# Kernel tuning notes

Hardware: AMD Instinct MI355X
Metric: run time of the kernel (lower is better)

## Reference

```python
import jax, jax.numpy as jnp
import numpy as np

SIGMA_S = 1.0
SIGMA_R = 0.1
FR = int(np.ceil(3 * SIGMA_S))          # 3
K_SIZE = 2 * FR + 1                     # 7
B, C, H, W = 8, 3, 512, 512


def matlab_style_gauss2d(shape, sigma):
    m, n = [(ss - 1.0) / 2.0 for ss in shape]
    y, x = np.ogrid[-m:m + 1, -n:n + 1]
    h = np.exp(-(x * x + y * y) / (2.0 * sigma * sigma))
    h[h < np.finfo(h.dtype).eps * h.max()] = 0
    s = h.sum()
    if s != 0:
        h /= s
    return h.astype(np.float32)


GAUSS = matlab_style_gauss2d((K_SIZE, K_SIZE), SIGMA_S)  # [7,7]


def setup_inputs() -> dict:
    key = jax.random.key(0)
    x = jax.random.uniform(key, (B, C, H, W), dtype=jnp.float32)
    return {"input": x}


def reference(input) -> jnp.ndarray:
    # ReflectionPad2d(fr)
    padded = jnp.pad(input, ((0, 0), (0, 0), (FR, FR), (FR, FR)), mode="reflect")
    inv_2sr2 = 1.0 / (2.0 * SIGMA_R * SIGMA_R)
    loss_map = jnp.zeros_like(input)
    for k in range(K_SIZE):
        for l in range(K_SIZE):
            shifted = padded[:, :, k:k + H, l:l + W]            # [B,C,H,W]
            d = input - shifted
            # bilateral range weight * gaussian spatial weight (constant, as in
            # the original which stores weight_map as a raw non-grad tensor)
            w = jax.lax.stop_gradient(
                jnp.exp(-(d * d).sum(1, keepdims=True) * inv_2sr2) * GAUSS[k, l]
            )                                                    # [B,1,H,W]
            loss_map = loss_map + jnp.abs(d) * w
    return loss_map.mean()
```

## Files before the change

kernel.cpp:

```cpp
#include <hip/hip_runtime.h>

#define FR 3
#define KS 7
#define TLX 64
#define TLY 16
#define PPT 4
#define HX (TLX + 2*FR)
#define HY (TLY + 2*FR)
#define LSTR 72
#define IMG_H 512
#define IMG_W 512
#define NB 8
#define NC 3
#define GX (IMG_W / TLX)
#define GY (IMG_H / TLY)
#define NBLK (GX * GY * NB)

#define KSC 8.493218f

__device__ __forceinline__ int refl(int i, int n) {
    i = (i < 0) ? -i : i;
    return (i >= n) ? (2*n - 2 - i) : i;
}

__global__ __launch_bounds__(256) void blt_kernel(const float* __restrict__ in,
                                                  float* __restrict__ partial) {
    __shared__ float sm[NC][HY][LSTR];
    __shared__ float gtab[8];
    __shared__ float wsum[4];

    constexpr double g0 = 0.011108996538242306;
    constexpr double g1 = 0.1353352832366127;
    constexpr double g2 = 0.6065306597126334;
    constexpr double SUMG = 1.0 + 2.0 * (g0 + g1 + g2);
    constexpr double KD   = 8.493218;
    const float glc[KS] = {
        (float)(g0 / (SUMG * SUMG * KD)), (float)(g1 / (SUMG * SUMG * KD)),
        (float)(g2 / (SUMG * SUMG * KD)), (float)(1.0 / (SUMG * SUMG * KD)),
        (float)(g2 / (SUMG * SUMG * KD)), (float)(g1 / (SUMG * SUMG * KD)),
        (float)(g0 / (SUMG * SUMG * KD))
    };

    const int bx  = blockIdx.x * TLX;
    const int by  = blockIdx.y * TLY;
    const int b   = blockIdx.z;
    const int tx  = threadIdx.x;
    const int ty  = threadIdx.y;
    const int tid = ty * 64 + tx;
    const float* base = in + (size_t)b * NC * IMG_H * IMG_W;

    if (tid == 0) {
        gtab[0] = (float)g0; gtab[1] = (float)g1; gtab[2] = (float)g2;
        gtab[3] = 1.0f;      gtab[4] = (float)g2; gtab[5] = (float)g1;
        gtab[6] = (float)g0;
    }

    for (int idx = tid; idx < HY * HX; idx += 256) {
        int ly = idx / HX;
        int lx = idx - ly * HX;
        int gy = refl(by + ly - FR, IMG_H);
        int gx = refl(bx + lx - FR, IMG_W);
        #pragma unroll
        for (int c = 0; c < NC; ++c)
            sm[c][ly][lx] = base[(c * IMG_H + gy) * IMG_W + gx] * KSC;
    }
    __syncthreads();

    const int r0 = ty * PPT;
    float c0[PPT], c1[PPT], c2[PPT], acc[PPT];
    #pragma unroll
    for (int i = 0; i < PPT; ++i) {
        c0[i] = sm[0][r0 + i + FR][tx + FR];
        c1[i] = sm[1][r0 + i + FR][tx + FR];
        c2[i] = sm[2][r0 + i + FR][tx + FR];
        acc[i] = 0.0f;
    }

    #pragma unroll 1
    for (int r = 0; r < PPT + KS - 1; ++r) {
        const int hr = r0 + r;
        float v0[KS], v1[KS], v2[KS];
        #pragma unroll
        for (int l = 0; l < KS; ++l) {
            v0[l] = sm[0][hr][tx + l];
            v1[l] = sm[1][hr][tx + l];
            v2[l] = sm[2][hr][tx + l];
        }
        #pragma unroll
        for (int i = 0; i < PPT; ++i) {
            const int k = r - i;
            if (k < 0 || k >= KS) continue;
            float t = 0.0f;
            #pragma unroll
            for (int l = 0; l < KS; ++l) {
                float d0 = c0[i] - v0[l];
                float d1 = c1[i] - v1[l];
                float d2 = c2[i] - v2[l];
                float s = d0 * d0;
                s = fmaf(d1, d1, s);
                s = fmaf(d2, d2, s);
                float e = __builtin_amdgcn_exp2f(-s);
                float sa = fabsf(d0) + fabsf(d1);
                sa += fabsf(d2);
                t = fmaf(sa, e * glc[l], t);
            }
            acc[i] = fmaf(t, gtab[k], acc[i]);
        }
    }

    float a = acc[0] + acc[1] + acc[2] + acc[3];
    #pragma unroll
    for (int off = 32; off > 0; off >>= 1)
        a += __shfl_down(a, off, 64);
    if ((tid & 63) == 0) wsum[tid >> 6] = a;
    __syncthreads();
    if (tid == 0) {
        int bid = blockIdx.x + GX * (blockIdx.y + GY * blockIdx.z);
        partial[bid] = wsum[0] + wsum[1] + wsum[2] + wsum[3];
    }
}

__global__ __launch_bounds__(256) void finalize_kernel(const float* __restrict__ partial,
                                                       float* __restrict__ out) {
    __shared__ float wsum[4];
    const int tid = threadIdx.x;
    float a = 0.0f;
    for (int i = tid; i < NBLK; i += 256) a += partial[i];
    #pragma unroll
    for (int off = 32; off > 0; off >>= 1)
        a += __shfl_down(a, off, 64);
    if ((tid & 63) == 0) wsum[tid >> 6] = a;
    __syncthreads();
    if (tid == 0)
        out[0] = (wsum[0] + wsum[1] + wsum[2] + wsum[3]) / (float)(NB * NC * IMG_H * IMG_W);
}

extern "C" void kernel_launch(void* const* d_in, const int* in_sizes, int n_in,
                              void* d_out, int out_size, void* d_ws, size_t ws_size,
                              hipStream_t stream) {
    const float* in = (const float*)d_in[0];
    float* out = (float*)d_out;
    float* ws  = (float*)d_ws;

    dim3 grid(GX, GY, NB);
    dim3 block(TLX, 256 / TLX);
    blt_kernel<<<grid, block, 0, stream>>>(in, ws);
    finalize_kernel<<<1, 256, 0, stream>>>(ws, out);
}
```

Baseline: 107.2 us.

## Exploit pair symmetry to halve bilateral work and handle reflected rim separately

The main kernel now evaluates only half of the 7x7 neighbourhood (upper rows plus the left half of the centre row) and doubles the weight, since |d|·w is symmetric for in-image pixel pairs. Out-of-image neighbours are masked out, and a new rim kernel adds the terms from the reflected padding for the 3-pixel border. This cuts the exp and arithmetic count roughly in half and shrinks the shared halo. In exchange it adds a third launch with scattered, uncoalesced gathers for the border pixels, and the row loop is fully unrolled, which raises register pressure.

New measurement: 98.49 us. 8.1% less time.

```diff
diff --git a/kernel.cpp b/kernel.cpp
--- a/kernel.cpp
+++ b/kernel.cpp
@@ -6,40 +6,41 @@
 #define TLY 16
 #define PPT 4
 #define HX (TLX + 2*FR)
-#define HY (TLY + 2*FR)
+#define HY (TLY + FR)
 #define LSTR 72
 #define IMG_H 512
 #define IMG_W 512
 #define NB 8
 #define NC 3
-#define GX (IMG_W / TLX)
-#define GY (IMG_H / TLY)
-#define NBLK (GX * GY * NB)
+#define GXB (IMG_W / TLX)
+#define GYB (IMG_H / TLY)
+#define NMAIN (GXB * GYB * NB)
+#define RIM_PER_IMG 6108
+#define NRIM_THREADS (RIM_PER_IMG * NB)
+#define NRIM_BLK ((NRIM_THREADS + 255) / 256)
+#define NPART (NMAIN + NRIM_BLK)
 
 #define KSC 8.493218f
+#define K2F 72.134752f
+
+constexpr double g1d[KS] = {0.011108996538242306, 0.1353352832366127,
+                            0.6065306597126334,   1.0,
+                            0.6065306597126334,   0.1353352832366127,
+                            0.011108996538242306};
+constexpr double SUMG = 1.0 + 2.0 * (0.011108996538242306 + 0.1353352832366127
+                                     + 0.6065306597126334);
+constexpr double INVN = 1.0 / (SUMG * SUMG);
+constexpr double KD   = 8.493218;
 
 __device__ __forceinline__ int refl(int i, int n) {
     i = (i < 0) ? -i : i;
     return (i >= n) ? (2*n - 2 - i) : i;
 }
 
-__global__ __launch_bounds__(256) void blt_kernel(const float* __restrict__ in,
-                                                  float* __restrict__ partial) {
+__global__ __launch_bounds__(256) void blt_main(const float* __restrict__ in,
+                                                float* __restrict__ partial) {
     __shared__ float sm[NC][HY][LSTR];
-    __shared__ float gtab[8];
     __shared__ float wsum[4];
-
-    constexpr double g0 = 0.011108996538242306;
-    constexpr double g1 = 0.1353352832366127;
-    constexpr double g2 = 0.6065306597126334;
-    constexpr double SUMG = 1.0 + 2.0 * (g0 + g1 + g2);
-    constexpr double KD   = 8.493218;
-    const float glc[KS] = {
-        (float)(g0 / (SUMG * SUMG * KD)), (float)(g1 / (SUMG * SUMG * KD)),
-        (float)(g2 / (SUMG * SUMG * KD)), (float)(1.0 / (SUMG * SUMG * KD)),
-        (float)(g2 / (SUMG * SUMG * KD)), (float)(g1 / (SUMG * SUMG * KD)),
-        (float)(g0 / (SUMG * SUMG * KD))
-    };
 
     const int bx  = blockIdx.x * TLX;
     const int by  = blockIdx.y * TLY;
@@ -49,12 +50,6 @@
     const int tid = ty * 64 + tx;
     const float* base = in + (size_t)b * NC * IMG_H * IMG_W;
 
-    if (tid == 0) {
-        gtab[0] = (float)g0; gtab[1] = (float)g1; gtab[2] = (float)g2;
-        gtab[3] = 1.0f;      gtab[4] = (float)g2; gtab[5] = (float)g1;
-        gtab[6] = (float)g0;
-    }
-
     for (int idx = tid; idx < HY * HX; idx += 256) {
         int ly = idx / HX;
         int lx = idx - ly * HX;
@@ -66,7 +61,19 @@
     }
     __syncthreads();
 
+    float glm[KS];
+    #pragma unroll
+    for (int l = 0; l < KS; ++l) {
+        bool inx = (unsigned)(bx + tx + l - FR) < (unsigned)IMG_W;
+        glm[l] = inx ? (float)(2.0 * g1d[l] * INVN / KD) : 0.0f;
+    }
+
     const int r0 = ty * PPT;
+    float gym[KS];
+    #pragma unroll
+    for (int rr = 0; rr < KS; ++rr)
+        gym[rr] = (by + r0 + rr - FR >= 0) ? 1.0f : 0.0f;
+
     float c0[PPT], c1[PPT], c2[PPT], acc[PPT];
     #pragma unroll
     for (int i = 0; i < PPT; ++i) {
@@ -76,23 +83,24 @@
         acc[i] = 0.0f;
     }
 
-    #pragma unroll 1
-    for (int r = 0; r < PPT + KS - 1; ++r) {
-        const int hr = r0 + r;
+    #pragma unroll
+    for (int rr = 0; rr < KS; ++rr) {
         float v0[KS], v1[KS], v2[KS];
         #pragma unroll
         for (int l = 0; l < KS; ++l) {
-            v0[l] = sm[0][hr][tx + l];
-            v1[l] = sm[1][hr][tx + l];
-            v2[l] = sm[2][hr][tx + l];
+            v0[l] = sm[0][r0 + rr][tx + l];
+            v1[l] = sm[1][r0 + rr][tx + l];
+            v2[l] = sm[2][r0 + rr][tx + l];
         }
         #pragma unroll
         for (int i = 0; i < PPT; ++i) {
-            const int k = r - i;
-            if (k < 0 || k >= KS) continue;
+            const int k = rr - i;
+            if (k < 0 || k > FR) continue;
+            const int lmax = (k == FR) ? FR : KS;
             float t = 0.0f;
             #pragma unroll
-            for (int l = 0; l < KS; ++l) {
+            for (int l = 0; l < 7; ++l) {
+                if (l >= lmax) continue;
                 float d0 = c0[i] - v0[l];
                 float d1 = c1[i] - v1[l];
                 float d2 = c2[i] - v2[l];
@@ -102,9 +110,9 @@
                 float e = __builtin_amdgcn_exp2f(-s);
                 float sa = fabsf(d0) + fabsf(d1);
                 sa += fabsf(d2);
-                t = fmaf(sa, e * glc[l], t);
+                t = fmaf(sa, e * glm[l], t);
             }
-            acc[i] = fmaf(t, gtab[k], acc[i]);
+            acc[i] = fmaf(t, (float)g1d[k] * gym[rr], acc[i]);
         }
     }
 
@@ -115,9 +123,61 @@
     if ((tid & 63) == 0) wsum[tid >> 6] = a;
     __syncthreads();
     if (tid == 0) {
-        int bid = blockIdx.x + GX * (blockIdx.y + GY * blockIdx.z);
+        int bid = blockIdx.x + GXB * (blockIdx.y + GYB * blockIdx.z);
         partial[bid] = wsum[0] + wsum[1] + wsum[2] + wsum[3];
     }
+}
+
+__global__ __launch_bounds__(256) void blt_rim(const float* __restrict__ in,
+                                               float* __restrict__ partial) {
+    __shared__ float wsum[4];
+    const int tid = threadIdx.x;
+    const int idx = blockIdx.x * 256 + tid;
+    float a = 0.0f;
+    if (idx < NRIM_THREADS) {
+        const int b = idx / RIM_PER_IMG;
+        int r = idx - b * RIM_PER_IMG;
+        int y, x;
+        if (r < 3 * IMG_W) { y = r >> 9; x = r & (IMG_W - 1); }
+        else if (r < 6 * IMG_W) { r -= 3 * IMG_W; y = (IMG_H - 3) + (r >> 9); x = r & (IMG_W - 1); }
+        else if (r < 6 * IMG_W + 3 * (IMG_H - 6)) { r -= 6 * IMG_W; y = 3 + r / 3; x = r - 3 * (r / 3); }
+        else { r -= 6 * IMG_W + 3 * (IMG_H - 6); y = 3 + r / 3; x = (IMG_W - 3) + (r - 3 * (r / 3)); }
+
+        const float* base = in + (size_t)b * NC * IMG_H * IMG_W;
+        const float cc0 = base[(0 * IMG_H + y) * IMG_W + x];
+        const float cc1 = base[(1 * IMG_H + y) * IMG_W + x];
+        const float cc2 = base[(2 * IMG_H + y) * IMG_W + x];
+
+        #pragma unroll
+        for (int k = 0; k < KS; ++k) {
+            #pragma unroll
+            for (int l = 0; l < KS; ++l) {
+                if (k == FR && l == FR) continue;
+                const int dy = k - FR, dx = l - FR;
+                int qy = y + dy, qx = x + dx;
+                bool oob = ((unsigned)qy >= (unsigned)IMG_H) | ((unsigned)qx >= (unsigned)IMG_W);
+                if (oob) {
+                    int ry = refl(qy, IMG_H), rx = refl(qx, IMG_W);
+                    float v0 = base[(0 * IMG_H + ry) * IMG_W + rx];
+                    float v1 = base[(1 * IMG_H + ry) * IMG_W + rx];
+                    float v2 = base[(2 * IMG_H + ry) * IMG_W + rx];
+                    float d0 = cc0 - v0, d1 = cc1 - v1, d2 = cc2 - v2;
+                    float s = d0 * d0;
+                    s = fmaf(d1, d1, s);
+                    s = fmaf(d2, d2, s);
+                    float e = __builtin_amdgcn_exp2f(-(K2F * s));
+                    float sa = fabsf(d0) + fabsf(d1) + fabsf(d2);
+                    a = fmaf(sa, e * (float)(g1d[k] * g1d[l] * INVN), a);
+                }
+            }
+        }
+    }
+    #pragma unroll
+    for (int off = 32; off > 0; off >>= 1)
+        a += __shfl_down(a, off, 64);
+    if ((tid & 63) == 0) wsum[tid >> 6] = a;
+    __syncthreads();
+    if (tid == 0) partial[NMAIN + blockIdx.x] = wsum[0] + wsum[1] + wsum[2] + wsum[3];
 }
 
 __global__ __launch_bounds__(256) void finalize_kernel(const float* __restrict__ partial,
@@ -125,7 +185,7 @@
     __shared__ float wsum[4];
     const int tid = threadIdx.x;
     float a = 0.0f;
-    for (int i = tid; i < NBLK; i += 256) a += partial[i];
+    for (int i = tid; i < NPART; i += 256) a += partial[i];
     #pragma unroll
     for (int off = 32; off > 0; off >>= 1)
         a += __shfl_down(a, off, 64);
@@ -142,8 +202,9 @@
     float* out = (float*)d_out;
     float* ws  = (float*)d_ws;
 
-    dim3 grid(GX, GY, NB);
+    dim3 grid(GXB, GYB, NB);
     dim3 block(TLX, 256 / TLX);
-    blt_kernel<<<grid, block, 0, stream>>>(in, ws);
+    blt_main<<<grid, block, 0, stream>>>(in, ws);
+    blt_rim<<<NRIM_BLK, 256, 0, stream>>>(in, ws);
     finalize_kernel<<<1, 256, 0, stream>>>(ws, out);
 }
```
